# Performance work log

Hardware: AMD Instinct MI355X
Metric: run time of the kernel (lower is better)

Reference implementation:

```python
import jax, jax.numpy as jnp
import numpy as np
import math

# ---------- helpers ----------

def conv(x, w, b=None, pad=1):
    y = jax.lax.conv_general_dilated(x, w, (1, 1), [(pad, pad), (pad, pad)],
                                     dimension_numbers=('NCHW', 'OIHW', 'NCHW'))
    return y if b is None else y + b[None, :, None, None]


def bn(x, g, b, m, v, eps=1e-5):
    scale = (g / jnp.sqrt(v + eps))[None, :, None, None]
    return (x - m[None, :, None, None]) * scale + b[None, :, None, None]


def _interp(x, axis, out_size):
    # bilinear resize along one axis with align_corners=True semantics
    n = x.shape[axis]
    c = jnp.arange(out_size, dtype=jnp.float32) * (n - 1) / (out_size - 1)
    lo = jnp.floor(c).astype(jnp.int32)
    hi = jnp.minimum(lo + 1, n - 1)
    w = c - lo
    xl = jnp.take(x, lo, axis=axis)
    xh = jnp.take(x, hi, axis=axis)
    wshape = [1] * x.ndim
    wshape[axis] = out_size
    w = w.reshape(wshape)
    return xl * (1.0 - w) + xh * w


def upsample2x(x):
    B, C, H, W = x.shape
    return _interp(_interp(x, 2, 2 * H), 3, 2 * W)


def haar_dwt2d(x):
    # single-level orthonormal haar DWT; equivalent to the per-(b,c) dwt2d loop,
    # vectorized over batch and channel via strided slicing
    a = x[..., 0::2, 0::2]
    b = x[..., 0::2, 1::2]
    c = x[..., 1::2, 0::2]
    d = x[..., 1::2, 1::2]
    LL = (a + b + c + d) * 0.5
    LH = (-a - b + c + d) * 0.5  # horizontal detail (row differences)
    HL = (-a + b - c + d) * 0.5  # vertical detail (col differences)
    HH = (a - b - c + d) * 0.5
    return LL, LH, HL, HH


def gabor_kernels(k=7, sigma=4.0, lambd=10.0, gamma=0.5, psi=0.0):
    thetas = jnp.array([0.0, math.pi / 4, math.pi / 2, 3 * math.pi / 4], dtype=jnp.float32)
    r = jnp.arange(-(k // 2), k // 2 + 1, dtype=jnp.float32)
    y, x = jnp.meshgrid(r, r, indexing='ij')

    def one(theta):
        xt = x * jnp.cos(theta) + y * jnp.sin(theta)
        yt = -x * jnp.sin(theta) + y * jnp.cos(theta)
        return jnp.exp(-0.5 * (xt ** 2 / sigma ** 2 + yt ** 2 / (sigma / gamma) ** 2)) \
               * jnp.cos(2.0 * math.pi * xt / lambd + psi)

    return jax.vmap(one)(thetas)[:, None]  # [4,1,k,k]


def cbam(x, fc1_w, fc2_w, sp_w):
    avg = x.mean(axis=(2, 3))
    mx = x.max(axis=(2, 3))
    mlp = lambda v: jax.nn.relu(v @ fc1_w.T) @ fc2_w.T
    ca = jax.nn.sigmoid(mlp(avg) + mlp(mx))[:, :, None, None]
    x = x * ca
    sp = jnp.concatenate([x.mean(axis=1, keepdims=True), x.max(axis=1, keepdims=True)], axis=1)
    sa = jax.nn.sigmoid(conv(sp, sp_w, pad=3))
    return x * sa


# ---------- inputs ----------

def setup_inputs() -> dict:
    B, Cin, Cout, H, W = 16, 64, 64, 128, 128
    Cr = Cout // 16
    ks = jax.random.split(jax.random.key(0), 32)
    p = lambda k, s, sc=0.05: jax.random.normal(k, s, dtype=jnp.float32) * sc
    g = lambda k, c: 1.0 + 0.1 * jax.random.normal(k, (c,), dtype=jnp.float32)
    return {
        'x': jax.random.normal(ks[0], (B, Cin, H, W), dtype=jnp.float32),
        'conv_in_w': p(ks[1], (Cout, Cin, 3, 3)),
        'bn1_g': g(ks[2], Cout), 'bn1_b': p(ks[3], (Cout,)),
        'bn1_m': p(ks[4], (Cout,)), 'bn1_v': jax.random.uniform(ks[5], (Cout,), minval=0.5, maxval=1.5),
        'down1_w': p(ks[6], (1, Cout, 3, 3)), 'down1_b': p(ks[7], (1,)),
        'down2_w': p(ks[8], (1, Cout, 3, 3)), 'down2_b': p(ks[9], (1,)),
        'wt_w': p(ks[10], (1, 1, 3, 3)), 'wt_b': p(ks[11], (1,)),
        'edge_w': p(ks[12], (Cout, 1, 3, 3)), 'edge_b': p(ks[13], (Cout,)),
        'up_w': p(ks[14], (Cout, 2, 3, 3)),
        'bn2_g': g(ks[15], Cout), 'bn2_b': p(ks[16], (Cout,)),
        'bn2_m': p(ks[17], (Cout,)), 'bn2_v': jax.random.uniform(ks[18], (Cout,), minval=0.5, maxval=1.5),
        'combine_w': p(ks[19], (Cout, 2 * Cout, 3, 3)), 'combine_b': p(ks[20], (Cout,)),
        'cbam_fc1_w': p(ks[21], (Cr, Cout)), 'cbam_fc2_w': p(ks[22], (Cout, Cr)),
        'cbam_sp_w': p(ks[23], (1, 2, 7, 7)),
        'out_w': p(ks[24], (Cout, Cout, 3, 3)),
        'bn3_g': g(ks[25], Cout), 'bn3_b': p(ks[26], (Cout,)),
        'bn3_m': p(ks[27], (Cout,)), 'bn3_v': jax.random.uniform(ks[28], (Cout,), minval=0.5, maxval=1.5),
    }


def reference(x, conv_in_w, bn1_g, bn1_b, bn1_m, bn1_v, down1_w, down1_b,
              down2_w, down2_b, wt_w, wt_b, edge_w, edge_b, up_w,
              bn2_g, bn2_b, bn2_m, bn2_v, combine_w, combine_b,
              cbam_fc1_w, cbam_fc2_w, cbam_sp_w, out_w,
              bn3_g, bn3_b, bn3_m, bn3_v):
    x1 = jax.nn.relu(bn(conv(x, conv_in_w), bn1_g, bn1_b, bn1_m, bn1_v))   # BasicConv2d
    X = upsample2x(x1)                                                      # [B,C,2H,2W]
    x_in = conv(x1, down1_w, down1_b)                                       # [B,1,H,W]
    X_in = conv(X, down2_w, down2_b)                                        # [B,1,2H,2W]
    cA, cH, cV, cD = haar_dwt2d(X_in)                                       # [B,1,H,W] each
    edge = conv(jnp.abs(cH) + jnp.abs(cV) + jnp.abs(cD), edge_w, edge_b)    # [B,C,H,W]
    gk = gabor_kernels()                                                    # all 4 thetas in one conv
    gab = jax.nn.sigmoid(conv(x_in, gk, pad=3).mean(axis=1, keepdims=True))
    wt = conv(cA, wt_w, wt_b)
    fusion = jax.nn.relu(bn(conv(jnp.concatenate([wt, gab], axis=1), up_w),
                            bn2_g, bn2_b, bn2_m, bn2_v))
    fusion = conv(jnp.concatenate([fusion, edge * (x1 + 1.0)], axis=1), combine_w, combine_b)
    att = cbam(fusion, cbam_fc1_w, cbam_fc2_w, cbam_sp_w)
    return jax.nn.relu(bn(conv(att, out_w), bn3_g, bn3_b, bn3_m, bn3_v))
```

## Files before the change

kernel.cpp:

```cpp
#include <hip/hip_runtime.h>
#include <math.h>

#define HWc 16384
#define Wd 128
#define Hd 128

typedef __attribute__((ext_vector_type(8))) _Float16 half8;
typedef __attribute__((ext_vector_type(4))) _Float16 half4;
typedef __attribute__((ext_vector_type(4))) float f32x4;

__global__ void prep_wfrag_kernel(const float* __restrict__ w,
                                  _Float16* __restrict__ wf, int cin)
{
    int total = cin * 576;
    int idx = blockIdx.x * 256 + threadIdx.x;
    if (idx >= total) return;
    int KC = cin >> 5;
    int j = idx & 7;
    int lane = (idx >> 3) & 63;
    int rest = idx >> 9;
    int ot = rest & 3;
    int rest2 = rest >> 2;
    int kc = rest2 % KC;
    int t = rest2 / KC;
    int oc = ot * 16 + (lane & 15);
    int ci = kc * 32 + ((lane >> 4) << 3) + j;
    wf[idx] = (_Float16)w[((size_t)oc * cin + ci) * 9 + t];
}

__global__ __launch_bounds__(256) void pack4_kernel(const float* __restrict__ in,
                                                    _Float16* __restrict__ outp)
{
    int idx = blockIdx.x * 256 + threadIdx.x;
    int b = idx >> 14, p = idx & 16383;
    #pragma unroll
    for (int g4 = 0; g4 < 16; g4++) {
        half4 v;
        #pragma unroll
        for (int k = 0; k < 4; k++)
            v[k] = (_Float16)in[((size_t)b * 64 + g4 * 4 + k) * HWc + p];
        *(half4*)&outp[(((size_t)b * 16 + g4) * HWc + p) * 4] = v;
    }
}

__global__ __launch_bounds__(256) void mfma_conv64_kernel(
    const _Float16* __restrict__ inp4, const _Float16* __restrict__ wf,
    const float* __restrict__ bng, const float* __restrict__ bnb,
    const float* __restrict__ bnm, const float* __restrict__ bnv,
    const float* __restrict__ samul, const float* __restrict__ camul,
    _Float16* __restrict__ outp4, float* __restrict__ out32)
{
    __shared__ __align__(16) _Float16 slds[20736];
    __shared__ float sc[64], sh[64], caf[64];
    __shared__ float satile[324];
    int tid = threadIdx.x;
    int b = blockIdx.y;
    int tileid = blockIdx.x;
    int th = tileid >> 3, tw = tileid & 7;
    int h0 = th * 16 - 1, w0 = tw * 16 - 1;
    if (tid < 64) {
        float inv = rsqrtf(bnv[tid] + 1e-5f);
        float s = bng[tid] * inv;
        sc[tid] = s;
        sh[tid] = bnb[tid] - bnm[tid] * s;
        caf[tid] = camul ? camul[b * 64 + tid] : 1.0f;
    }
    if (samul) {
        const float* sp = samul + (size_t)b * HWc;
        for (int i = tid; i < 324; i += 256) {
            int y = i / 18, x = i - (i / 18) * 18;
            int hh = h0 + y, ww = w0 + x;
            satile[i] = (hh >= 0 && hh < Hd && ww >= 0 && ww < Wd) ? sp[hh * Wd + ww] : 0.f;
        }
    }
    __syncthreads();
    const _Float16* ib = inp4 + (size_t)b * 16 * HWc * 4;
    for (int i = tid; i < 2592; i += 256) {
        int g = i / 324;
        int rem = i - g * 324;
        int y = rem / 18, x = rem - (rem / 18) * 18;
        int hh = h0 + y, ww = w0 + x;
        half8 hv;
        if (hh >= 0 && hh < Hd && ww >= 0 && ww < Wd) {
            int p = hh * Wd + ww;
            half4 a = *(const half4*)&ib[((size_t)(2 * g) * HWc + p) * 4];
            half4 c = *(const half4*)&ib[((size_t)(2 * g + 1) * HWc + p) * 4];
            if (samul) {
                float m = satile[y * 18 + x];
                #pragma unroll
                for (int k = 0; k < 4; k++) {
                    hv[k]     = (_Float16)((float)a[k] * caf[g * 8 + k] * m);
                    hv[k + 4] = (_Float16)((float)c[k] * caf[g * 8 + 4 + k] * m);
                }
            } else {
                #pragma unroll
                for (int k = 0; k < 4; k++) { hv[k] = a[k]; hv[k + 4] = c[k]; }
            }
        } else {
            #pragma unroll
            for (int k = 0; k < 8; k++) hv[k] = (_Float16)0.f;
        }
        *(half8*)&slds[i * 8] = hv;
    }
    __syncthreads();
    int lane = tid & 63, wid = tid >> 6;
    int lq = lane >> 4, ln = lane & 15;
    int y0 = wid * 4;
    f32x4 acc[4][4];
    #pragma unroll
    for (int r = 0; r < 4; r++)
        #pragma unroll
        for (int ot = 0; ot < 4; ot++)
            #pragma unroll
            for (int q = 0; q < 4; q++) acc[r][ot][q] = 0.f;

    for (int t = 0; t < 9; t++) {
        int dy = t / 3, dx = t - (t / 3) * 3;
        #pragma unroll
        for (int kc = 0; kc < 2; kc++) {
            half8 bf[4];
            #pragma unroll
            for (int r = 0; r < 4; r++) {
                int off = (((kc * 4 + lq) * 324) + (y0 + r + dy) * 18 + (ln + dx)) * 8;
                bf[r] = *(const half8*)&slds[off];
            }
            #pragma unroll
            for (int ot = 0; ot < 4; ot++) {
                half8 af = *(const half8*)(wf + (size_t)(((t * 2 + kc) * 4 + ot) * 64 + lane) * 8);
                #pragma unroll
                for (int r = 0; r < 4; r++)
                    acc[r][ot] = __builtin_amdgcn_mfma_f32_16x16x32_f16(af, bf[r], acc[r][ot], 0, 0, 0);
            }
        }
    }
    #pragma unroll
    for (int r = 0; r < 4; r++) {
        int yy = th * 16 + y0 + r;
        int p = yy * Wd + tw * 16 + ln;
        #pragma unroll
        for (int ot = 0; ot < 4; ot++) {
            int g4 = ot * 4 + lq;
            if (out32) {
                #pragma unroll
                for (int reg = 0; reg < 4; reg++) {
                    int oc = g4 * 4 + reg;
                    float v = fmaf(acc[r][ot][reg], sc[oc], sh[oc]);
                    out32[((size_t)b * 64 + oc) * HWc + p] = fmaxf(v, 0.f);
                }
            } else {
                half4 hv;
                #pragma unroll
                for (int reg = 0; reg < 4; reg++) {
                    int oc = g4 * 4 + reg;
                    float v = fmaf(acc[r][ot][reg], sc[oc], sh[oc]);
                    hv[reg] = (_Float16)fmaxf(v, 0.f);
                }
                *(half4*)&outp4[(((size_t)b * 16 + g4) * HWc + p) * 4] = hv;
            }
        }
    }
}

__global__ __launch_bounds__(256) void mfma_combine_kernel(
    const _Float16* __restrict__ f1p, const float* __restrict__ Ein,
    const _Float16* __restrict__ x1p,
    const float* __restrict__ edge_w, const float* __restrict__ edge_b,
    const _Float16* __restrict__ wf, const float* __restrict__ cb,
    _Float16* __restrict__ outp4)
{
    __shared__ __align__(16) _Float16 slds[20736];
    __shared__ float e20[400];
    __shared__ float ew[576];
    __shared__ float ebl[64];
    __shared__ float cbl[64];
    int tid = threadIdx.x;
    int b = blockIdx.y;
    int tileid = blockIdx.x;
    int th = tileid >> 3, tw = tileid & 7;
    int h0 = th * 16 - 1, w0 = tw * 16 - 1;
    {
        const float* ep = Ein + (size_t)b * HWc;
        for (int i = tid; i < 400; i += 256) {
            int y = i / 20, x = i - (i / 20) * 20;
            int hh = h0 - 1 + y, ww = w0 - 1 + x;
            e20[i] = (hh >= 0 && hh < Hd && ww >= 0 && ww < Wd) ? ep[hh * Wd + ww] : 0.f;
        }
        for (int i = tid; i < 576; i += 256) ew[i] = edge_w[i];
        if (tid < 64) { ebl[tid] = edge_b[tid]; cbl[tid] = cb[tid]; }
    }
    int lane = tid & 63, wid = tid >> 6;
    int lq = lane >> 4, ln = lane & 15;
    int y0 = wid * 4;
    f32x4 acc[4][4];
    #pragma unroll
    for (int r = 0; r < 4; r++)
        #pragma unroll
        for (int ot = 0; ot < 4; ot++)
            #pragma unroll
            for (int q = 0; q < 4; q++) acc[r][ot][q] = 0.f;

    const _Float16* f1b = f1p + (size_t)b * 16 * HWc * 4;
    const _Float16* x1b = x1p + (size_t)b * 16 * HWc * 4;
    for (int h = 0; h < 2; h++) {
        __syncthreads();
        if (h == 0) {
            for (int i = tid; i < 2592; i += 256) {
                int g = i / 324;
                int rem = i - g * 324;
                int y = rem / 18, x = rem - (rem / 18) * 18;
                int hh = h0 + y, ww = w0 + x;
                half8 hv;
                if (hh >= 0 && hh < Hd && ww >= 0 && ww < Wd) {
                    int p = hh * Wd + ww;
                    half4 a = *(const half4*)&f1b[((size_t)(2 * g) * HWc + p) * 4];
                    half4 c = *(const half4*)&f1b[((size_t)(2 * g + 1) * HWc + p) * 4];
                    #pragma unroll
                    for (int k = 0; k < 4; k++) { hv[k] = a[k]; hv[k + 4] = c[k]; }
                } else {
                    #pragma unroll
                    for (int k = 0; k < 8; k++) hv[k] = (_Float16)0.f;
                }
                *(half8*)&slds[i * 8] = hv;
            }
        } else {
            for (int i = tid; i < 2592; i += 256) {
                int g = i / 324;
                int rem = i - g * 324;
                int y = rem / 18, x = rem - (rem / 18) * 18;
                int hh = h0 + y, ww = w0 + x;
                half8 hv;
                if (hh >= 0 && hh < Hd && ww >= 0 && ww < Wd) {
                    int p = hh * Wd + ww;
                    float e[9];
                    #pragma unroll
                    for (int tt = 0; tt < 9; tt++)
                        e[tt] = e20[(y + tt / 3) * 20 + x + (tt - (tt / 3) * 3)];
                    half4 a = *(const half4*)&x1b[((size_t)(2 * g) * HWc + p) * 4];
                    half4 c = *(const half4*)&x1b[((size_t)(2 * g + 1) * HWc + p) * 4];
                    #pragma unroll
                    for (int k = 0; k < 8; k++) {
                        int cc = g * 8 + k;
                        float ec = ebl[cc];
                        #pragma unroll
                        for (int tt = 0; tt < 9; tt++) ec = fmaf(ew[cc * 9 + tt], e[tt], ec);
                        float xv = (k < 4) ? (float)a[k] : (float)c[k - 4];
                        hv[k] = (_Float16)(ec * (xv + 1.0f));
                    }
                } else {
                    #pragma unroll
                    for (int k = 0; k < 8; k++) hv[k] = (_Float16)0.f;
                }
                *(half8*)&slds[i * 8] = hv;
            }
        }
        __syncthreads();
        for (int t = 0; t < 9; t++) {
            int dy = t / 3, dx = t - (t / 3) * 3;
            #pragma unroll
            for (int kc = 0; kc < 2; kc++) {
                int kcg = h * 2 + kc;
                half8 bf[4];
                #pragma unroll
                for (int r = 0; r < 4; r++) {
                    int off = (((kc * 4 + lq) * 324) + (y0 + r + dy) * 18 + (ln + dx)) * 8;
                    bf[r] = *(const half8*)&slds[off];
                }
                #pragma unroll
                for (int ot = 0; ot < 4; ot++) {
                    half8 af = *(const half8*)(wf + (size_t)(((t * 4 + kcg) * 4 + ot) * 64 + lane) * 8);
                    #pragma unroll
                    for (int r = 0; r < 4; r++)
                        acc[r][ot] = __builtin_amdgcn_mfma_f32_16x16x32_f16(af, bf[r], acc[r][ot], 0, 0, 0);
                }
            }
        }
    }
    #pragma unroll
    for (int r = 0; r < 4; r++) {
        int yy = th * 16 + y0 + r;
        int p = yy * Wd + tw * 16 + ln;
        #pragma unroll
        for (int ot = 0; ot < 4; ot++) {
            int g4 = ot * 4 + lq;
            half4 hv;
            #pragma unroll
            for (int reg = 0; reg < 4; reg++) {
                int oc = g4 * 4 + reg;
                hv[reg] = (_Float16)(acc[r][ot][reg] + cbl[oc]);
            }
            *(half4*)&outp4[(((size_t)b * 16 + g4) * HWc + p) * 4] = hv;
        }
    }
}

__global__ __launch_bounds__(256) void conv3x3_bn_kernel(
    const float* __restrict__ in, const float* __restrict__ wgt,
    const float* __restrict__ bng, const float* __restrict__ bnb,
    const float* __restrict__ bnm, const float* __restrict__ bnv,
    _Float16* __restrict__ outp4, int cin)
{
    __shared__ float tile[18*18];
    __shared__ float wl[576];
    __shared__ float sc[64], sh[64];
    int tid = threadIdx.x;
    int tileid = blockIdx.x; int b = blockIdx.y;
    int th = tileid >> 3, tw = tileid & 7;
    int h0 = th*16 - 1, w0 = tw*16 - 1;
    if (tid < 64) {
        float inv = rsqrtf(bnv[tid] + 1e-5f);
        float s = bng[tid]*inv;
        sc[tid] = s;
        sh[tid] = bnb[tid] - bnm[tid]*s;
    }
    float acc[64];
    #pragma unroll
    for (int i=0;i<64;i++) acc[i]=0.f;
    int py = tid>>4, px = tid&15;
    for (int ci=0; ci<cin; ci++){
        __syncthreads();
        const float* inp = in + ((size_t)b*cin + ci)*HWc;
        for (int i = tid; i < 324; i += 256) {
            int y=i/18, x=i%18; int hh=h0+y, ww=w0+x;
            tile[i] = (hh>=0&&hh<Hd&&ww>=0&&ww<Wd) ? inp[hh*Wd+ww] : 0.f;
        }
        for (int i = tid; i < 576; i += 256) {
            int oc = i/9, t = i - oc*9;
            wl[i] = wgt[((size_t)oc*cin + ci)*9 + t];
        }
        __syncthreads();
        float v[9];
        #pragma unroll
        for (int dy=0;dy<3;dy++)
            #pragma unroll
            for (int dx=0;dx<3;dx++)
                v[dy*3+dx] = tile[(py+dy)*18 + px+dx];
        #pragma unroll
        for (int oc=0;oc<64;oc++){
            float a = acc[oc];
            #pragma unroll
            for (int t=0;t<9;t++) a = fmaf(wl[oc*9+t], v[t], a);
            acc[oc]=a;
        }
    }
    int hh = h0+1+py, ww = w0+1+px;
    int p = hh*Wd + ww;
    #pragma unroll
    for (int g4=0; g4<16; g4++){
        half4 hv;
        #pragma unroll
        for (int reg=0; reg<4; reg++){
            int oc = g4*4+reg;
            float y = fmaf(acc[oc], sc[oc], sh[oc]);
            hv[reg] = (_Float16)fmaxf(y, 0.f);
        }
        *(half4*)&outp4[(((size_t)b*16+g4)*HWc + p)*4] = hv;
    }
}

__global__ __launch_bounds__(256) void zmaps_kernel(const _Float16* __restrict__ x1p,
    const float* __restrict__ w2, const float* __restrict__ w1,
    float* __restrict__ z, float* __restrict__ z1)
{
    int idx = blockIdx.x*256 + threadIdx.x;
    int b = idx >> 14; int p = idx & 16383;
    const _Float16* xb = x1p + (size_t)b*16*HWc*4;
    float a2[9], a1[9];
    #pragma unroll
    for (int t=0;t<9;t++){ a2[t]=0.f; a1[t]=0.f; }
    for (int g4=0; g4<16; g4++){
        half4 v = *(const half4*)&xb[((size_t)g4*HWc + p)*4];
        #pragma unroll
        for (int k=0;k<4;k++){
            int c = g4*4+k;
            float val = (float)v[k];
            #pragma unroll
            for (int t=0;t<9;t++){
                a2[t] = fmaf(w2[c*9+t], val, a2[t]);
                a1[t] = fmaf(w1[c*9+t], val, a1[t]);
            }
        }
    }
    #pragma unroll
    for (int t=0;t<9;t++){
        z [((size_t)b*9+t)*HWc + p] = a2[t];
        z1[((size_t)b*9+t)*HWc + p] = a1[t];
    }
}

__global__ __launch_bounds__(256) void xin_kernel(const float* __restrict__ z1,
    const float* __restrict__ b1p, float* __restrict__ xin)
{
    int idx = blockIdx.x*256+threadIdx.x;
    int b=idx>>14; int p=idx&16383;
    int i=p>>7, j=p&127;
    float acc = b1p[0];
    #pragma unroll
    for (int t=0;t<9;t++){
        int ii=i+t/3-1, jj=j+t%3-1;
        if (ii>=0&&ii<Hd&&jj>=0&&jj<Wd)
            acc += z1[((size_t)b*9+t)*HWc + ii*Wd+jj];
    }
    xin[idx]=acc;
}

__global__ __launch_bounds__(256) void dwt_kernel(const float* __restrict__ z,
    const float* __restrict__ b2p, float* __restrict__ cA, float* __restrict__ Eo)
{
    int idx = blockIdx.x*256 + threadIdx.x;
    int b = idx >> 14; int p = idx & 16383;
    int u = p >> 7, v = p & 127;
    float b2 = b2p[0];
    int rlo[4], rhi[4]; float rf[4]; bool rv[4];
    int clo[4], chi[4]; float cf[4]; bool cvv[4];
    #pragma unroll
    for (int k=0;k<4;k++){
        int r = 2*u - 1 + k;
        rv[k] = (r>=0 && r<256);
        int rr = rv[k] ? r : 0;
        float cc = ((float)rr * 127.0f) / 255.0f;
        int lo = (int)cc;
        rlo[k]=lo; rhi[k]=min(lo+1,127); rf[k]=cc-(float)lo;
        int s = 2*v - 1 + k;
        cvv[k] = (s>=0 && s<256);
        int ss = cvv[k] ? s : 0;
        float c2 = ((float)ss * 127.0f) / 255.0f;
        int lo2=(int)c2;
        clo[k]=lo2; chi[k]=min(lo2+1,127); cf[k]=c2-(float)lo2;
    }
    float Xin[4] = {b2,b2,b2,b2};
    #pragma unroll
    for (int t=0;t<9;t++){
        int dy=t/3, dx=t%3;
        const float* zp = z + ((size_t)b*9 + t)*HWc;
        #pragma unroll
        for (int e=0;e<4;e++){
            int ey=e>>1, ex=e&1;
            int k=ey+dy, l=ex+dx;
            if (rv[k] && cvv[l]){
                const float* row0 = zp + rlo[k]*Wd;
                const float* row1 = zp + rhi[k]*Wd;
                float v00=row0[clo[l]], v01=row0[chi[l]];
                float v10=row1[clo[l]], v11=row1[chi[l]];
                float fc_=cf[l], fr_=rf[k];
                float top = v00*(1.0f-fc_) + v01*fc_;
                float bot = v10*(1.0f-fc_) + v11*fc_;
                Xin[e] += top*(1.0f-fr_) + bot*fr_;
            }
        }
    }
    float a=Xin[0], bb=Xin[1], c_=Xin[2], d_=Xin[3];
    float LL=0.5f*( a+bb+c_+d_);
    float LH=0.5f*(-a-bb+c_+d_);
    float HL=0.5f*(-a+bb-c_+d_);
    float HH=0.5f*( a-bb-c_+d_);
    cA[(size_t)b*HWc + p] = LL;
    Eo[(size_t)b*HWc + p] = fabsf(LH)+fabsf(HL)+fabsf(HH);
}

__global__ __launch_bounds__(256) void wtgab_kernel(const float* __restrict__ cA,
    const float* __restrict__ xin, const float* __restrict__ wtw, const float* __restrict__ wtb,
    float* __restrict__ wtgab)
{
    __shared__ float gm[49];
    int tid=threadIdx.x;
    if (tid<49){
        int ky=tid/7, kx=tid%7;
        float yy=(float)(ky-3), xx=(float)(kx-3);
        float s=0.f;
        for (int t=0;t<4;t++){
            float theta = (float)t * 0.7853981633974483f;
            float ct=cosf(theta), st=sinf(theta);
            float xt = xx*ct + yy*st;
            float yt = -xx*st + yy*ct;
            s += expf(-0.5f*(xt*xt*(1.0f/16.0f) + yt*yt*(1.0f/64.0f))) * cosf(0.6283185307179586f*xt);
        }
        gm[tid]=0.25f*s;
    }
    __syncthreads();
    int idx = blockIdx.x*256+tid;
    int b=idx>>14; int p=idx&16383;
    int i=p>>7, j=p&127;
    float wacc = wtb[0];
    #pragma unroll
    for (int t=0;t<9;t++){
        int ii=i+t/3-1, jj=j+t%3-1;
        if (ii>=0&&ii<Hd&&jj>=0&&jj<Wd)
            wacc = fmaf(wtw[t], cA[b*HWc + ii*Wd+jj], wacc);
    }
    float g=0.f;
    for (int k=0;k<49;k++){
        int ii=i+k/7-3, jj=j+k%7-3;
        if (ii>=0&&ii<Hd&&jj>=0&&jj<Wd)
            g = fmaf(gm[k], xin[b*HWc + ii*Wd+jj], g);
    }
    wtgab[((size_t)b*2)*HWc + p] = wacc;
    wtgab[((size_t)b*2+1)*HWc + p] = 1.0f/(1.0f+expf(-g));
}

__global__ __launch_bounds__(256) void pool_kernel(const _Float16* __restrict__ fp4,
    float* __restrict__ pavg, float* __restrict__ pmax)
{
    int b = blockIdx.x >> 4, g4 = blockIdx.x & 15;
    int tid = threadIdx.x;
    const _Float16* p = fp4 + ((size_t)b*16 + g4)*HWc*4;
    float s[4] = {0,0,0,0};
    float m[4] = {-3.4e38f,-3.4e38f,-3.4e38f,-3.4e38f};
    for (int i=tid;i<HWc;i+=256){
        half4 v = *(const half4*)&p[(size_t)i*4];
        #pragma unroll
        for (int k=0;k<4;k++){ float u=(float)v[k]; s[k]+=u; m[k]=fmaxf(m[k],u); }
    }
    __shared__ float ss[4][256], sm[4][256];
    #pragma unroll
    for (int k=0;k<4;k++){ ss[k][tid]=s[k]; sm[k][tid]=m[k]; }
    __syncthreads();
    for (int st=128; st>0; st>>=1){
        if (tid<st){
            #pragma unroll
            for (int k=0;k<4;k++){
                ss[k][tid]+=ss[k][tid+st];
                sm[k][tid]=fmaxf(sm[k][tid],sm[k][tid+st]);
            }
        }
        __syncthreads();
    }
    if (tid<4){
        pavg[b*64 + g4*4 + tid] = ss[tid][0]*(1.0f/16384.0f);
        pmax[b*64 + g4*4 + tid] = sm[tid][0];
    }
}

__global__ void mlp_kernel(const float* __restrict__ pavg, const float* __restrict__ pmax,
    const float* __restrict__ fc1, const float* __restrict__ fc2, float* __restrict__ ca)
{
    int b = blockIdx.x; int tid = threadIdx.x;
    __shared__ float hs[4];
    if (tid < 4){
        float sa_=0.f, sm_=0.f;
        for (int c=0;c<64;c++){
            float w = fc1[tid*64+c];
            sa_ = fmaf(w, pavg[b*64+c], sa_);
            sm_ = fmaf(w, pmax[b*64+c], sm_);
        }
        hs[tid] = fmaxf(sa_,0.f) + fmaxf(sm_,0.f);
    }
    __syncthreads();
    float o = 0.f;
    #pragma unroll
    for (int j=0;j<4;j++) o = fmaf(fc2[tid*4+j], hs[j], o);
    ca[b*64+tid] = 1.0f/(1.0f+expf(-o));
}

__global__ __launch_bounds__(256) void spstats_kernel(const _Float16* __restrict__ fp4,
    const float* __restrict__ ca, float* __restrict__ spmean, float* __restrict__ spmax)
{
    int idx = blockIdx.x*256+threadIdx.x;
    int b = idx>>14; int p = idx&16383;
    const _Float16* fb = fp4 + (size_t)b*16*HWc*4;
    const float* cp = ca + b*64;
    float s=0.f, m=-3.4e38f;
    for (int g4=0; g4<16; g4++){
        half4 v = *(const half4*)&fb[((size_t)g4*HWc + p)*4];
        #pragma unroll
        for (int k=0;k<4;k++){
            float u = (float)v[k] * cp[g4*4+k];
            s += u; m = fmaxf(m, u);
        }
    }
    spmean[idx] = s*(1.0f/64.0f);
    spmax[idx] = m;
}

__global__ __launch_bounds__(256) void spconv_kernel(const float* __restrict__ spmean,
    const float* __restrict__ spmax, const float* __restrict__ spw, float* __restrict__ sa)
{
    int idx = blockIdx.x*256+threadIdx.x;
    int b=idx>>14; int p=idx&16383;
    int i=p>>7, j=p&127;
    float acc=0.f;
    for (int k=0;k<49;k++){
        int ky=k/7-3, kx=k%7-3;
        int ii=i+ky, jj=j+kx;
        if (ii>=0&&ii<Hd&&jj>=0&&jj<Wd){
            int q = b*HWc + ii*Wd+jj;
            acc = fmaf(spw[k],    spmean[q], acc);
            acc = fmaf(spw[49+k], spmax[q], acc);
        }
    }
    sa[idx] = 1.0f/(1.0f+expf(-acc));
}

extern "C" void kernel_launch(void* const* d_in, const int* in_sizes, int n_in,
                              void* d_out, int out_size, void* d_ws, size_t ws_size,
                              hipStream_t stream)
{
    const float* x         = (const float*)d_in[0];
    const float* conv_in_w = (const float*)d_in[1];
    const float* bn1_g = (const float*)d_in[2];
    const float* bn1_b = (const float*)d_in[3];
    const float* bn1_m = (const float*)d_in[4];
    const float* bn1_v = (const float*)d_in[5];
    const float* down1_w = (const float*)d_in[6];
    const float* down1_b = (const float*)d_in[7];
    const float* down2_w = (const float*)d_in[8];
    const float* down2_b = (const float*)d_in[9];
    const float* wt_w = (const float*)d_in[10];
    const float* wt_b = (const float*)d_in[11];
    const float* edge_w = (const float*)d_in[12];
    const float* edge_b = (const float*)d_in[13];
    const float* up_w = (const float*)d_in[14];
    const float* bn2_g = (const float*)d_in[15];
    const float* bn2_b = (const float*)d_in[16];
    const float* bn2_m = (const float*)d_in[17];
    const float* bn2_v = (const float*)d_in[18];
    const float* combine_w = (const float*)d_in[19];
    const float* combine_b = (const float*)d_in[20];
    const float* fc1 = (const float*)d_in[21];
    const float* fc2 = (const float*)d_in[22];
    const float* spw = (const float*)d_in[23];
    const float* out_w = (const float*)d_in[24];
    const float* bn3_g = (const float*)d_in[25];
    const float* bn3_b = (const float*)d_in[26];
    const float* bn3_m = (const float*)d_in[27];
    const float* bn3_v = (const float*)d_in[28];
    float* out = (float*)d_out;
    float* ws = (float*)d_ws;

    float* z       = ws;
    float* z1      = z + 2359296;
    float* xin     = z1 + 2359296;
    float* cA      = xin + 262144;
    float* Ebuf    = cA + 262144;
    float* wtgab   = Ebuf + 262144;
    float* spmean  = wtgab + 524288;
    float* spmaxb  = spmean + 262144;
    float* sabuf   = spmaxb + 262144;
    float* pavg    = sabuf + 262144;
    float* pmaxb   = pavg + 1024;
    float* cab     = pmaxb + 1024;
    _Float16* xp      = (_Float16*)(cab + 1024);
    _Float16* x1p     = xp + 16777216;
    _Float16* f1p     = x1p + 16777216;
    _Float16* fp      = f1p + 16777216;
    _Float16* wf_in   = fp + 16777216;
    _Float16* wf_out  = wf_in + 36864;
    _Float16* wf_comb = wf_out + 36864;

    prep_wfrag_kernel<<<144, 256, 0, stream>>>(conv_in_w, wf_in, 64);
    prep_wfrag_kernel<<<144, 256, 0, stream>>>(out_w, wf_out, 64);
    prep_wfrag_kernel<<<288, 256, 0, stream>>>(combine_w, wf_comb, 128);
    pack4_kernel<<<1024, 256, 0, stream>>>(x, xp);

    dim3 cgrid(64, 16);
    mfma_conv64_kernel<<<cgrid, 256, 0, stream>>>(xp, wf_in, bn1_g,bn1_b,bn1_m,bn1_v,
                                                  nullptr, nullptr, x1p, nullptr);
    zmaps_kernel<<<1024, 256, 0, stream>>>(x1p, down2_w, down1_w, z, z1);
    xin_kernel<<<1024, 256, 0, stream>>>(z1, down1_b, xin);
    dwt_kernel<<<1024, 256, 0, stream>>>(z, down2_b, cA, Ebuf);
    wtgab_kernel<<<1024, 256, 0, stream>>>(cA, xin, wt_w, wt_b, wtgab);
    conv3x3_bn_kernel<<<cgrid, 256, 0, stream>>>(wtgab, up_w, bn2_g,bn2_b,bn2_m,bn2_v, f1p, 2);
    mfma_combine_kernel<<<cgrid, 256, 0, stream>>>(f1p, Ebuf, x1p, edge_w, edge_b,
                                                   wf_comb, combine_b, fp);
    pool_kernel<<<256, 256, 0, stream>>>(fp, pavg, pmaxb);
    mlp_kernel<<<16, 64, 0, stream>>>(pavg, pmaxb, fc1, fc2, cab);
    spstats_kernel<<<1024, 256, 0, stream>>>(fp, cab, spmean, spmaxb);
    spconv_kernel<<<1024, 256, 0, stream>>>(spmean, spmaxb, spw, sabuf);
    mfma_conv64_kernel<<<cgrid, 256, 0, stream>>>(fp, wf_out, bn3_g,bn3_b,bn3_m,bn3_v,
                                                  sabuf, cab, nullptr, out);
}
```

Before: 535.7 us.

## Read conv operands directly from global memory and split edge/attention modulation into prepasses

The MFMA conv and combine kernels no longer stage the halo tile in LDS. Each lane now loads its B-fragment straight from global memory, relying on the cache for the 9x reuse, and the kernels declare launch bounds of 4 blocks. The edge-conv times (x1+1) product and the channel/spatial attention scaling move out of the conv prologues into separate elementwise kernels, edgemul and modmul, which write fp16 intermediates into reused buffers. This removes LDS pressure and barriers to raise occupancy, but adds extra full-tensor passes and redundant global loads for each tap.

```diff
diff --git a/kernel.cpp b/kernel.cpp
--- a/kernel.cpp
+++ b/kernel.cpp
@@ -43,16 +43,13 @@
     }
 }
 
-__global__ __launch_bounds__(256) void mfma_conv64_kernel(
+__global__ __launch_bounds__(256, 4) void mfma_conv64_kernel(
     const _Float16* __restrict__ inp4, const _Float16* __restrict__ wf,
     const float* __restrict__ bng, const float* __restrict__ bnb,
     const float* __restrict__ bnm, const float* __restrict__ bnv,
-    const float* __restrict__ samul, const float* __restrict__ camul,
     _Float16* __restrict__ outp4, float* __restrict__ out32)
 {
-    __shared__ __align__(16) _Float16 slds[20736];
-    __shared__ float sc[64], sh[64], caf[64];
-    __shared__ float satile[324];
+    __shared__ float sc[64], sh[64];
     int tid = threadIdx.x;
     int b = blockIdx.y;
     int tileid = blockIdx.x;
@@ -63,46 +60,9 @@
         float s = bng[tid] * inv;
         sc[tid] = s;
         sh[tid] = bnb[tid] - bnm[tid] * s;
-        caf[tid] = camul ? camul[b * 64 + tid] : 1.0f;
-    }
-    if (samul) {
-        const float* sp = samul + (size_t)b * HWc;
-        for (int i = tid; i < 324; i += 256) {
-            int y = i / 18, x = i - (i / 18) * 18;
-            int hh = h0 + y, ww = w0 + x;
-            satile[i] = (hh >= 0 && hh < Hd && ww >= 0 && ww < Wd) ? sp[hh * Wd + ww] : 0.f;
-        }
     }
     __syncthreads();
     const _Float16* ib = inp4 + (size_t)b * 16 * HWc * 4;
-    for (int i = tid; i < 2592; i += 256) {
-        int g = i / 324;
-        int rem = i - g * 324;
-        int y = rem / 18, x = rem - (rem / 18) * 18;
-        int hh = h0 + y, ww = w0 + x;
-        half8 hv;
-        if (hh >= 0 && hh < Hd && ww >= 0 && ww < Wd) {
-            int p = hh * Wd + ww;
-            half4 a = *(const half4*)&ib[((size_t)(2 * g) * HWc + p) * 4];
-            half4 c = *(const half4*)&ib[((size_t)(2 * g + 1) * HWc + p) * 4];
-            if (samul) {
-                float m = satile[y * 18 + x];
-                #pragma unroll
-                for (int k = 0; k < 4; k++) {
-                    hv[k]     = (_Float16)((float)a[k] * caf[g * 8 + k] * m);
-                    hv[k + 4] = (_Float16)((float)c[k] * caf[g * 8 + 4 + k] * m);
-                }
-            } else {
-                #pragma unroll
-                for (int k = 0; k < 4; k++) { hv[k] = a[k]; hv[k + 4] = c[k]; }
-            }
-        } else {
-            #pragma unroll
-            for (int k = 0; k < 8; k++) hv[k] = (_Float16)0.f;
-        }
-        *(half8*)&slds[i * 8] = hv;
-    }
-    __syncthreads();
     int lane = tid & 63, wid = tid >> 6;
     int lq = lane >> 4, ln = lane & 15;
     int y0 = wid * 4;
@@ -116,13 +76,27 @@
 
     for (int t = 0; t < 9; t++) {
         int dy = t / 3, dx = t - (t / 3) * 3;
+        int ww = w0 + ln + dx;
+        bool wok = (ww >= 0 && ww < Wd);
         #pragma unroll
         for (int kc = 0; kc < 2; kc++) {
+            int g = kc * 4 + lq;
             half8 bf[4];
             #pragma unroll
             for (int r = 0; r < 4; r++) {
-                int off = (((kc * 4 + lq) * 324) + (y0 + r + dy) * 18 + (ln + dx)) * 8;
-                bf[r] = *(const half8*)&slds[off];
+                int hh = h0 + y0 + r + dy;
+                half8 hv;
+                if (wok && hh >= 0 && hh < Hd) {
+                    int p = hh * Wd + ww;
+                    half4 a = *(const half4*)&ib[((size_t)(2 * g) * HWc + p) * 4];
+                    half4 c = *(const half4*)&ib[((size_t)(2 * g + 1) * HWc + p) * 4];
+                    #pragma unroll
+                    for (int k = 0; k < 4; k++) { hv[k] = a[k]; hv[k + 4] = c[k]; }
+                } else {
+                    #pragma unroll
+                    for (int k = 0; k < 8; k++) hv[k] = (_Float16)0.f;
+                }
+                bf[r] = hv;
             }
             #pragma unroll
             for (int ot = 0; ot < 4; ot++) {
@@ -161,33 +135,19 @@
     }
 }
 
-__global__ __launch_bounds__(256) void mfma_combine_kernel(
-    const _Float16* __restrict__ f1p, const float* __restrict__ Ein,
-    const _Float16* __restrict__ x1p,
-    const float* __restrict__ edge_w, const float* __restrict__ edge_b,
+__global__ __launch_bounds__(256, 4) void mfma_combine_kernel(
+    const _Float16* __restrict__ f1p, const _Float16* __restrict__ emod,
     const _Float16* __restrict__ wf, const float* __restrict__ cb,
     _Float16* __restrict__ outp4)
 {
-    __shared__ __align__(16) _Float16 slds[20736];
-    __shared__ float e20[400];
-    __shared__ float ew[576];
-    __shared__ float ebl[64];
     __shared__ float cbl[64];
     int tid = threadIdx.x;
     int b = blockIdx.y;
     int tileid = blockIdx.x;
     int th = tileid >> 3, tw = tileid & 7;
     int h0 = th * 16 - 1, w0 = tw * 16 - 1;
-    {
-        const float* ep = Ein + (size_t)b * HWc;
-        for (int i = tid; i < 400; i += 256) {
-            int y = i / 20, x = i - (i / 20) * 20;
-            int hh = h0 - 1 + y, ww = w0 - 1 + x;
-            e20[i] = (hh >= 0 && hh < Hd && ww >= 0 && ww < Wd) ? ep[hh * Wd + ww] : 0.f;
-        }
-        for (int i = tid; i < 576; i += 256) ew[i] = edge_w[i];
-        if (tid < 64) { ebl[tid] = edge_b[tid]; cbl[tid] = cb[tid]; }
-    }
+    if (tid < 64) cbl[tid] = cb[tid];
+    __syncthreads();
     int lane = tid & 63, wid = tid >> 6;
     int lq = lane >> 4, ln = lane & 15;
     int y0 = wid * 4;
@@ -200,70 +160,33 @@
             for (int q = 0; q < 4; q++) acc[r][ot][q] = 0.f;
 
     const _Float16* f1b = f1p + (size_t)b * 16 * HWc * 4;
-    const _Float16* x1b = x1p + (size_t)b * 16 * HWc * 4;
+    const _Float16* emb = emod + (size_t)b * 16 * HWc * 4;
     for (int h = 0; h < 2; h++) {
-        __syncthreads();
-        if (h == 0) {
-            for (int i = tid; i < 2592; i += 256) {
-                int g = i / 324;
-                int rem = i - g * 324;
-                int y = rem / 18, x = rem - (rem / 18) * 18;
-                int hh = h0 + y, ww = w0 + x;
-                half8 hv;
-                if (hh >= 0 && hh < Hd && ww >= 0 && ww < Wd) {
-                    int p = hh * Wd + ww;
-                    half4 a = *(const half4*)&f1b[((size_t)(2 * g) * HWc + p) * 4];
-                    half4 c = *(const half4*)&f1b[((size_t)(2 * g + 1) * HWc + p) * 4];
-                    #pragma unroll
-                    for (int k = 0; k < 4; k++) { hv[k] = a[k]; hv[k + 4] = c[k]; }
-                } else {
-                    #pragma unroll
-                    for (int k = 0; k < 8; k++) hv[k] = (_Float16)0.f;
-                }
-                *(half8*)&slds[i * 8] = hv;
-            }
-        } else {
-            for (int i = tid; i < 2592; i += 256) {
-                int g = i / 324;
-                int rem = i - g * 324;
-                int y = rem / 18, x = rem - (rem / 18) * 18;
-                int hh = h0 + y, ww = w0 + x;
-                half8 hv;
-                if (hh >= 0 && hh < Hd && ww >= 0 && ww < Wd) {
-                    int p = hh * Wd + ww;
-                    float e[9];
-                    #pragma unroll
-                    for (int tt = 0; tt < 9; tt++)
-                        e[tt] = e20[(y + tt / 3) * 20 + x + (tt - (tt / 3) * 3)];
-                    half4 a = *(const half4*)&x1b[((size_t)(2 * g) * HWc + p) * 4];
-                    half4 c = *(const half4*)&x1b[((size_t)(2 * g + 1) * HWc + p) * 4];
-                    #pragma unroll
-                    for (int k = 0; k < 8; k++) {
-                        int cc = g * 8 + k;
-                        float ec = ebl[cc];
-                        #pragma unroll
-                        for (int tt = 0; tt < 9; tt++) ec = fmaf(ew[cc * 9 + tt], e[tt], ec);
-                        float xv = (k < 4) ? (float)a[k] : (float)c[k - 4];
-                        hv[k] = (_Float16)(ec * (xv + 1.0f));
-                    }
-                } else {
-                    #pragma unroll
-                    for (int k = 0; k < 8; k++) hv[k] = (_Float16)0.f;
-                }
-                *(half8*)&slds[i * 8] = hv;
-            }
-        }
-        __syncthreads();
+        const _Float16* src = (h == 0) ? f1b : emb;
         for (int t = 0; t < 9; t++) {
             int dy = t / 3, dx = t - (t / 3) * 3;
+            int ww = w0 + ln + dx;
+            bool wok = (ww >= 0 && ww < Wd);
             #pragma unroll
             for (int kc = 0; kc < 2; kc++) {
                 int kcg = h * 2 + kc;
+                int g = kc * 4 + lq;
                 half8 bf[4];
                 #pragma unroll
                 for (int r = 0; r < 4; r++) {
-                    int off = (((kc * 4 + lq) * 324) + (y0 + r + dy) * 18 + (ln + dx)) * 8;
-                    bf[r] = *(const half8*)&slds[off];
+                    int hh = h0 + y0 + r + dy;
+                    half8 hv;
+                    if (wok && hh >= 0 && hh < Hd) {
+                        int p = hh * Wd + ww;
+                        half4 a = *(const half4*)&src[((size_t)(2 * g) * HWc + p) * 4];
+                        half4 c = *(const half4*)&src[((size_t)(2 * g + 1) * HWc + p) * 4];
+                        #pragma unroll
+                        for (int k = 0; k < 4; k++) { hv[k] = a[k]; hv[k + 4] = c[k]; }
+                    } else {
+                        #pragma unroll
+                        for (int k = 0; k < 8; k++) hv[k] = (_Float16)0.f;
+                    }
+                    bf[r] = hv;
                 }
                 #pragma unroll
                 for (int ot = 0; ot < 4; ot++) {
@@ -290,6 +213,73 @@
             }
             *(half4*)&outp4[(((size_t)b * 16 + g4) * HWc + p) * 4] = hv;
         }
+    }
+}
+
+__global__ __launch_bounds__(256) void edgemul_kernel(const float* __restrict__ E,
+    const _Float16* __restrict__ x1p, const float* __restrict__ edge_w,
+    const float* __restrict__ edge_b, _Float16* __restrict__ emod)
+{
+    __shared__ float ew[576];
+    __shared__ float ebl[64];
+    int tid = threadIdx.x;
+    for (int i = tid; i < 576; i += 256) ew[i] = edge_w[i];
+    if (tid < 64) ebl[tid] = edge_b[tid];
+    __syncthreads();
+    int idx = blockIdx.x * 256 + tid;
+    int b = idx >> 14, p = idx & 16383;
+    int i = p >> 7, j = p & 127;
+    const float* ep = E + (size_t)b * HWc;
+    float e[9];
+    #pragma unroll
+    for (int tt = 0; tt < 9; tt++) {
+        int ii = i - 1 + tt / 3, jj = j - 1 + tt % 3;
+        e[tt] = (ii >= 0 && ii < Hd && jj >= 0 && jj < Wd) ? ep[ii * Wd + jj] : 0.f;
+    }
+    const _Float16* xb = x1p + (size_t)b * 16 * HWc * 4;
+    _Float16* ob = emod + (size_t)b * 16 * HWc * 4;
+    for (int g = 0; g < 8; g++) {
+        half4 a = *(const half4*)&xb[((size_t)(2 * g) * HWc + p) * 4];
+        half4 c = *(const half4*)&xb[((size_t)(2 * g + 1) * HWc + p) * 4];
+        half8 hv;
+        #pragma unroll
+        for (int k = 0; k < 8; k++) {
+            int cc = g * 8 + k;
+            float ec = ebl[cc];
+            #pragma unroll
+            for (int tt = 0; tt < 9; tt++) ec = fmaf(ew[cc * 9 + tt], e[tt], ec);
+            float xv = (k < 4) ? (float)a[k] : (float)c[k - 4];
+            hv[k] = (_Float16)(ec * (xv + 1.0f));
+        }
+        half4 lo, hi;
+        #pragma unroll
+        for (int k = 0; k < 4; k++) { lo[k] = hv[k]; hi[k] = hv[k + 4]; }
+        *(half4*)&ob[((size_t)(2 * g) * HWc + p) * 4] = lo;
+        *(half4*)&ob[((size_t)(2 * g + 1) * HWc + p) * 4] = hi;
+    }
+}
+
+__global__ __launch_bounds__(256) void modmul_kernel(const _Float16* __restrict__ fp4,
+    const float* __restrict__ ca, const float* __restrict__ sa,
+    _Float16* __restrict__ outm)
+{
+    int idx = blockIdx.x * 256 + threadIdx.x;
+    int b = idx >> 14, p = idx & 16383;
+    float m = sa[(size_t)b * HWc + p];
+    const float* cp = ca + b * 64;
+    const _Float16* fb = fp4 + (size_t)b * 16 * HWc * 4;
+    _Float16* ob = outm + (size_t)b * 16 * HWc * 4;
+    for (int g = 0; g < 8; g++) {
+        half4 a = *(const half4*)&fb[((size_t)(2 * g) * HWc + p) * 4];
+        half4 c = *(const half4*)&fb[((size_t)(2 * g + 1) * HWc + p) * 4];
+        half4 lo, hi;
+        #pragma unroll
+        for (int k = 0; k < 4; k++) {
+            lo[k] = (_Float16)((float)a[k] * cp[g * 8 + k] * m);
+            hi[k] = (_Float16)((float)c[k] * cp[g * 8 + 4 + k] * m);
+        }
+        *(half4*)&ob[((size_t)(2 * g) * HWc + p) * 4] = lo;
+        *(half4*)&ob[((size_t)(2 * g + 1) * HWc + p) * 4] = hi;
     }
 }
 
@@ -645,6 +635,8 @@
     _Float16* wf_in   = fp + 16777216;
     _Float16* wf_out  = wf_in + 36864;
     _Float16* wf_comb = wf_out + 36864;
+    _Float16* emod = xp;
+    _Float16* fmod = f1p;
 
     prep_wfrag_kernel<<<144, 256, 0, stream>>>(conv_in_w, wf_in, 64);
     prep_wfrag_kernel<<<144, 256, 0, stream>>>(out_w, wf_out, 64);
@@ -653,18 +645,19 @@
 
     dim3 cgrid(64, 16);
     mfma_conv64_kernel<<<cgrid, 256, 0, stream>>>(xp, wf_in, bn1_g,bn1_b,bn1_m,bn1_v,
-                                                  nullptr, nullptr, x1p, nullptr);
+                                                  x1p, nullptr);
     zmaps_kernel<<<1024, 256, 0, stream>>>(x1p, down2_w, down1_w, z, z1);
     xin_kernel<<<1024, 256, 0, stream>>>(z1, down1_b, xin);
     dwt_kernel<<<1024, 256, 0, stream>>>(z, down2_b, cA, Ebuf);
     wtgab_kernel<<<1024, 256, 0, stream>>>(cA, xin, wt_w, wt_b, wtgab);
     conv3x3_bn_kernel<<<cgrid, 256, 0, stream>>>(wtgab, up_w, bn2_g,bn2_b,bn2_m,bn2_v, f1p, 2);
-    mfma_combine_kernel<<<cgrid, 256, 0, stream>>>(f1p, Ebuf, x1p, edge_w, edge_b,
-                                                   wf_comb, combine_b, fp);
+    edgemul_kernel<<<1024, 256, 0, stream>>>(Ebuf, x1p, edge_w, edge_b, emod);
+    mfma_combine_kernel<<<cgrid, 256, 0, stream>>>(f1p, emod, wf_comb, combine_b, fp);
     pool_kernel<<<256, 256, 0, stream>>>(fp, pavg, pmaxb);
     mlp_kernel<<<16, 64, 0, stream>>>(pavg, pmaxb, fc1, fc2, cab);
     spstats_kernel<<<1024, 256, 0, stream>>>(fp, cab, spmean, spmaxb);
     spconv_kernel<<<1024, 256, 0, stream>>>(spmean, spmaxb, spw, sabuf);
-    mfma_conv64_kernel<<<cgrid, 256, 0, stream>>>(fp, wf_out, bn3_g,bn3_b,bn3_m,bn3_v,
-                                                  sabuf, cab, nullptr, out);
-}
+    modmul_kernel<<<1024, 256, 0, stream>>>(fp, cab, sabuf, fmod);
+    mfma_conv64_kernel<<<cgrid, 256, 0, stream>>>(fmod, wf_out, bn3_g,bn3_b,bn3_m,bn3_v,
+                                                  nullptr, out);
+}
```

New measurement: 820.4 us. 53.2% more time.
